# Optimization experiments

Measured on AMD Instinct MI355X. Metric: run time of the kernel, lower is better.

## Reference

```python
import jax, jax.numpy as jnp
import numpy as np

N_TOKENS = 8192
D_MODEL = 1024
HIDDEN = 4096   # d_model * expert_hidden_mult(4)
N_EXPERTS = 8
TOP_K = 2
LN_EPS = 1e-5


def setup_inputs() -> dict:
    key = jax.random.key(0)
    ks = jax.random.split(key, 8)
    s_in = 1.0 / np.sqrt(D_MODEL)
    s_h = 1.0 / np.sqrt(HIDDEN)
    return {
        "x": jax.random.normal(ks[0], (N_TOKENS, D_MODEL), jnp.float32),
        "Wr": jax.random.normal(ks[1], (D_MODEL, N_EXPERTS), jnp.float32) * s_in,
        "W1": jax.random.normal(ks[2], (N_EXPERTS, D_MODEL, HIDDEN), jnp.float32) * s_in,
        "b1": jnp.zeros((N_EXPERTS, HIDDEN), jnp.float32),
        "W2": jax.random.normal(ks[3], (N_EXPERTS, HIDDEN, D_MODEL), jnp.float32) * s_h,
        "b2": jnp.zeros((N_EXPERTS, D_MODEL), jnp.float32),
        "ln_w": jnp.ones((D_MODEL,), jnp.float32),
        "ln_b": jnp.zeros((D_MODEL,), jnp.float32),
    }


def reference(x, Wr, W1, b1, W2, b2, ln_w, ln_b):
    N, d = x.shape
    E = Wr.shape[1]
    # --- Router: top-k softmax gates scattered into dense [N, E] ---
    logits = x @ Wr                                   # [N, E]
    topv, topi = jax.lax.top_k(logits, TOP_K)         # [N, K]
    gv = jax.nn.softmax(topv, axis=-1)                # renormalized top-k gates
    gates = jnp.zeros_like(logits).at[jnp.arange(N)[:, None], topi].set(gv)
    # --- Experts: gate_e > 0 masks tokens; zero gate contributes zero, so
    # dense per-expert FFN weighted by the (mostly-zero) gate column is the
    # same math as the original gather/FFN/scatter-add dispatch. ---
    mixed = jnp.zeros_like(x)
    for e in range(E):  # small fixed expert count
        h = jax.nn.gelu(x @ W1[e] + b1[e])            # [N, HIDDEN]
        y = h @ W2[e] + b2[e]                         # [N, d]
        mixed = mixed + gates[:, e:e + 1] * y
    # --- Load-balancing aux loss (importance * load) ---
    importance = jnp.mean(jax.nn.softmax(logits, axis=-1), axis=0)  # [E]
    load = jnp.mean((gates > 0).astype(x.dtype), axis=0)            # [E]
    aux_loss = E * jnp.sum(importance * load)
    # --- Residual + LayerNorm (output_dropout is identity in eval) ---
    res = x + mixed
    mu = jnp.mean(res, axis=-1, keepdims=True)
    var = jnp.var(res, axis=-1, keepdims=True)
    out = (res - mu) * jax.lax.rsqrt(var + LN_EPS) * ln_w + ln_b
    return out, aux_loss
```

## Files before the change

kernel.cpp:

```cpp
#include <hip/hip_runtime.h>

#define N_TOK 8192
#define DM 1024
#define HID 4096
#define NE 8
#define MAX_TILES 136
#define MAX_SLOTS (MAX_TILES * 128)
#define LN_EPS 1e-5f

typedef __attribute__((ext_vector_type(8))) _Float16 f16x8;
typedef __attribute__((ext_vector_type(4))) _Float16 f16x4;
typedef __attribute__((ext_vector_type(4))) float f32x4;

constexpr size_t OFF_WT1 = 0;
constexpr size_t OFF_WT2 = OFF_WT1 + (size_t)NE * HID * DM * 2;
constexpr size_t OFF_XG  = OFF_WT2 + (size_t)NE * DM * HID * 2;
constexpr size_t OFF_H   = OFF_XG + (size_t)MAX_SLOTS * DM * 2;
constexpr size_t OFF_Y   = OFF_H + (size_t)MAX_SLOTS * HID * 2;
constexpr size_t OFF_TOPI = OFF_Y + (size_t)MAX_SLOTS * DM * 2;
constexpr size_t OFF_TOPG = OFF_TOPI + (size_t)N_TOK * 2 * 4;
constexpr size_t OFF_PTOK = OFF_TOPG + (size_t)N_TOK * 2 * 4;
constexpr size_t OFF_SLOT = OFF_PTOK + (size_t)MAX_SLOTS * 4;
constexpr size_t OFF_HDR = OFF_SLOT + (size_t)N_TOK * 2 * 4;
constexpr size_t WS_NEEDED = OFF_HDR + 4096;

__device__ inline float gelu_tanh(float v) {
  float c = 0.7978845608028654f * (v + 0.044715f * v * v * v);
  return 0.5f * v * (1.0f + tanhf(c));
}

__device__ inline void g2l16(const _Float16* g, _Float16* l) {
  __builtin_amdgcn_global_load_lds(
      (const __attribute__((address_space(1))) unsigned int*)g,
      (__attribute__((address_space(3))) unsigned int*)l, 16, 0, 0);
}

__global__ __launch_bounds__(256) void k_router(
    const float* __restrict__ x, const float* __restrict__ Wr,
    int* __restrict__ topi, float* __restrict__ topg,
    int* __restrict__ cnt, float* __restrict__ imp) {
  __shared__ float wr[DM * NE];
  __shared__ float blkImp[NE];
  __shared__ int blkCnt[NE];
  int tid = threadIdx.x;
  if (tid < NE) { blkImp[tid] = 0.0f; blkCnt[tid] = 0; }
  for (int i = tid; i < DM * NE / 4; i += 256)
    ((float4*)wr)[i] = ((const float4*)Wr)[i];
  __syncthreads();
  int wave = tid >> 6, lane = tid & 63;
  for (int it = 0; it < 4; ++it) {
    int t = blockIdx.x * 16 + wave * 4 + it;
    double acc[NE];
#pragma unroll
    for (int e = 0; e < NE; ++e) acc[e] = 0.0;
    for (int j = 0; j < DM / 64; ++j) {
      int d = j * 64 + lane;
      float xv = x[(size_t)t * DM + d];
#pragma unroll
      for (int e = 0; e < NE; ++e) acc[e] += (double)xv * (double)wr[d * NE + e];
    }
#pragma unroll
    for (int off = 32; off > 0; off >>= 1) {
#pragma unroll
      for (int e = 0; e < NE; ++e) acc[e] += __shfl_down(acc[e], off);
    }
    if (lane == 0) {
      int i0 = 0;
#pragma unroll
      for (int e = 1; e < NE; ++e) if (acc[e] > acc[i0]) i0 = e;
      int i1 = (i0 == 0) ? 1 : 0;
#pragma unroll
      for (int e = 0; e < NE; ++e) if (e != i0 && acc[e] > acc[i1]) i1 = e;
      double g0 = 1.0 / (1.0 + exp(acc[i1] - acc[i0]));
      topi[t * 2] = i0; topi[t * 2 + 1] = i1;
      topg[t * 2] = (float)g0; topg[t * 2 + 1] = (float)(1.0 - g0);
      atomicAdd(&blkCnt[i0], 1); atomicAdd(&blkCnt[i1], 1);
      double mx = acc[0];
#pragma unroll
      for (int e = 1; e < NE; ++e) mx = acc[e] > mx ? acc[e] : mx;
      double s = 0.0, p[NE];
#pragma unroll
      for (int e = 0; e < NE; ++e) { p[e] = exp(acc[e] - mx); s += p[e]; }
      double inv = 1.0 / s;
#pragma unroll
      for (int e = 0; e < NE; ++e) atomicAdd(&blkImp[e], (float)(p[e] * inv));
    }
  }
  __syncthreads();
  if (tid < NE) { atomicAdd(&cnt[tid], blkCnt[tid]); atomicAdd(&imp[tid], blkImp[tid]); }
}

__global__ void k_setup(int* __restrict__ hdr, float* __restrict__ aux_out) {
  int* cnt = hdr;
  float* imp = (float*)(hdr + 8);
  int* cursor = hdr + 16;
  int* off = hdr + 24;
  int* n_tiles_p = hdr + 33;
  int* tile_expert = hdr + 34;
  if (threadIdx.x == 0) {
    int offl[NE + 1];
    int o = 0;
    for (int e = 0; e < NE; ++e) {
      offl[e] = o; off[e] = o; cursor[e] = o;
      o += ((cnt[e] + 127) >> 7) << 7;
    }
    offl[NE] = o; off[NE] = o;
    int nt = o >> 7;
    *n_tiles_p = nt;
    int e = 0;
    for (int i = 0; i < nt; ++i) {
      while (i * 128 >= offl[e + 1]) ++e;
      tile_expert[i] = e;
    }
    double a = 0.0;
    for (int e2 = 0; e2 < NE; ++e2)
      a += ((double)imp[e2] / (double)N_TOK) * ((double)cnt[e2] / (double)N_TOK);
    *aux_out = (float)((double)NE * a);
  }
}

__global__ __launch_bounds__(256) void k_init_pairs(int* __restrict__ pair_token) {
  int i = blockIdx.x * 256 + threadIdx.x;
  if (i < MAX_SLOTS) pair_token[i] = -1;
}

__global__ __launch_bounds__(256) void k_scatter(
    const int* __restrict__ topi, int* __restrict__ cursor,
    int* __restrict__ pair_token, int* __restrict__ slot_of) {
  int t = blockIdx.x * 256 + threadIdx.x;
#pragma unroll
  for (int k = 0; k < 2; ++k) {
    int e = topi[t * 2 + k];
    int p = atomicAdd(&cursor[e], 1);
    pair_token[p] = t;
    slot_of[t * 2 + k] = p;
  }
}

__global__ __launch_bounds__(256) void k_gather(
    const float* __restrict__ x, const int* __restrict__ pair_token,
    _Float16* __restrict__ Xg) {
  int slot = blockIdx.x;
  int t = pair_token[slot];
  int d = threadIdx.x * 4;
  f16x4 v4 = {0, 0, 0, 0};
  if (t >= 0) {
    float4 v = *(const float4*)(x + (size_t)t * DM + d);
    v4[0] = (_Float16)v.x; v4[1] = (_Float16)v.y;
    v4[2] = (_Float16)v.z; v4[3] = (_Float16)v.w;
  }
  *(f16x4*)(Xg + (size_t)slot * DM + d) = v4;
}

__global__ __launch_bounds__(256) void k_transpose(
    const float* __restrict__ in, _Float16* __restrict__ out, int R, int C) {
  __shared__ float tile[32][33];
  size_t base = (size_t)blockIdx.z * R * C;
  const float* src = in + base;
  _Float16* dst = out + base;
  int c0 = blockIdx.x * 32, r0 = blockIdx.y * 32;
  int tx = threadIdx.x & 31, ty = threadIdx.x >> 5;
#pragma unroll
  for (int i = 0; i < 32; i += 8)
    tile[ty + i][tx] = src[(size_t)(r0 + ty + i) * C + c0 + tx];
  __syncthreads();
#pragma unroll
  for (int i = 0; i < 32; i += 8)
    dst[(size_t)(c0 + ty + i) * R + r0 + tx] = (_Float16)tile[tx][ty + i];
}

__device__ inline void stage_async(const _Float16* __restrict__ g, int ld,
                                   _Float16* __restrict__ l, int tid) {
  int wbase = tid & 192;
#pragma unroll
  for (int p = 0; p < 4; ++p) {
    int s = p * 256 + tid;
    int row = s >> 3;
    int c = (s & 7) ^ (row & 7);
    g2l16(g + (size_t)row * ld + c * 8, l + (size_t)(p * 256 + wbase) * 8);
  }
}

__device__ inline f16x8 lds_frag(const _Float16* __restrict__ l, int row, int cc) {
  return *(const f16x8*)(l + row * 64 + (((cc) ^ (row & 7)) << 3));
}

__global__ __launch_bounds__(256, 4) void k_gemm1(
    const _Float16* __restrict__ Xg, const _Float16* __restrict__ Wt1,
    const float* __restrict__ b1, _Float16* __restrict__ H,
    const int* __restrict__ hdr) {
  int tileM = blockIdx.y;
  if (tileM >= hdr[33]) return;
  int e = hdr[34 + tileM];
  int tileN = blockIdx.x;
  __shared__ _Float16 Al[128 * 64];
  __shared__ _Float16 Bl[128 * 64];
  int tid = threadIdx.x;
  const _Float16* Ag = Xg + (size_t)tileM * 128 * DM;
  const _Float16* Bg = Wt1 + (size_t)e * HID * DM + (size_t)tileN * 128 * DM;
  f32x4 acc[4][4];
  const f32x4 fz = {0.f, 0.f, 0.f, 0.f};
#pragma unroll
  for (int a = 0; a < 4; ++a)
#pragma unroll
    for (int b = 0; b < 4; ++b) acc[a][b] = fz;
  int wave = tid >> 6, lane = tid & 63;
  int wm = wave & 1, wn = wave >> 1;
  int l16 = lane & 15, quad = lane >> 4;
  for (int k0 = 0; k0 < DM; k0 += 64) {
    stage_async(Ag + k0, DM, Al, tid);
    stage_async(Bg + k0, DM, Bl, tid);
    __syncthreads();
#pragma unroll
    for (int kk = 0; kk < 64; kk += 32) {
      f16x8 af[4], bfr[4];
      int cc = quad + (kk >> 3);
#pragma unroll
      for (int mi = 0; mi < 4; ++mi)
        af[mi] = lds_frag(Al, wm * 64 + mi * 16 + l16, cc);
#pragma unroll
      for (int ni = 0; ni < 4; ++ni)
        bfr[ni] = lds_frag(Bl, wn * 64 + ni * 16 + l16, cc);
#pragma unroll
      for (int mi = 0; mi < 4; ++mi)
#pragma unroll
        for (int ni = 0; ni < 4; ++ni)
          acc[mi][ni] = __builtin_amdgcn_mfma_f32_16x16x32_f16(af[mi], bfr[ni], acc[mi][ni], 0, 0, 0);
    }
    __syncthreads();
  }
  int rowBase = tileM * 128 + wm * 64;
  int colBase = tileN * 128 + wn * 64;
#pragma unroll
  for (int ni = 0; ni < 4; ++ni) {
    int col = colBase + ni * 16 + l16;
    float bv = b1[e * HID + col];
#pragma unroll
    for (int mi = 0; mi < 4; ++mi)
#pragma unroll
      for (int i = 0; i < 4; ++i) {
        int row = rowBase + mi * 16 + quad * 4 + i;
        float v = acc[mi][ni][i] + bv;
        H[(size_t)row * HID + col] = (_Float16)gelu_tanh(v);
      }
  }
}

__global__ __launch_bounds__(256, 4) void k_gemm2(
    const _Float16* __restrict__ H, const _Float16* __restrict__ Wt2,
    const float* __restrict__ b2, _Float16* __restrict__ Y,
    const int* __restrict__ hdr) {
  int tileM = blockIdx.y;
  if (tileM >= hdr[33]) return;
  int e = hdr[34 + tileM];
  int tileN = blockIdx.x;
  __shared__ _Float16 Al[128 * 64];
  __shared__ _Float16 Bl[128 * 64];
  int tid = threadIdx.x;
  const _Float16* Ag = H + (size_t)tileM * 128 * HID;
  const _Float16* Bg = Wt2 + (size_t)e * DM * HID + (size_t)tileN * 128 * HID;
  f32x4 acc[4][4];
  const f32x4 fz = {0.f, 0.f, 0.f, 0.f};
#pragma unroll
  for (int a = 0; a < 4; ++a)
#pragma unroll
    for (int b = 0; b < 4; ++b) acc[a][b] = fz;
  int wave = tid >> 6, lane = tid & 63;
  int wm = wave & 1, wn = wave >> 1;
  int l16 = lane & 15, quad = lane >> 4;
  for (int k0 = 0; k0 < HID; k0 += 64) {
    stage_async(Ag + k0, HID, Al, tid);
    stage_async(Bg + k0, HID, Bl, tid);
    __syncthreads();
#pragma unroll
    for (int kk = 0; kk < 64; kk += 32) {
      f16x8 af[4], bfr[4];
      int cc = quad + (kk >> 3);
#pragma unroll
      for (int mi = 0; mi < 4; ++mi)
        af[mi] = lds_frag(Al, wm * 64 + mi * 16 + l16, cc);
#pragma unroll
      for (int ni = 0; ni < 4; ++ni)
        bfr[ni] = lds_frag(Bl, wn * 64 + ni * 16 + l16, cc);
#pragma unroll
      for (int mi = 0; mi < 4; ++mi)
#pragma unroll
        for (int ni = 0; ni < 4; ++ni)
          acc[mi][ni] = __builtin_amdgcn_mfma_f32_16x16x32_f16(af[mi], bfr[ni], acc[mi][ni], 0, 0, 0);
    }
    __syncthreads();
  }
  int rowBase = tileM * 128 + wm * 64;
  int colBase = tileN * 128 + wn * 64;
#pragma unroll
  for (int ni = 0; ni < 4; ++ni) {
    int col = colBase + ni * 16 + l16;
    float bv = b2[e * DM + col];
#pragma unroll
    for (int mi = 0; mi < 4; ++mi)
#pragma unroll
      for (int i = 0; i < 4; ++i) {
        int row = rowBase + mi * 16 + quad * 4 + i;
        Y[(size_t)row * DM + col] = (_Float16)(acc[mi][ni][i] + bv);
      }
  }
}

__global__ __launch_bounds__(256) void k_ln(
    const float* __restrict__ x, const _Float16* __restrict__ Y,
    const int* __restrict__ slot_of, const float* __restrict__ topg,
    const float* __restrict__ lnw, const float* __restrict__ lnb,
    float* __restrict__ out) {
  int t = blockIdx.x, tid = threadIdx.x;
  int s0 = slot_of[t * 2], s1 = slot_of[t * 2 + 1];
  float g0 = topg[t * 2], g1 = topg[t * 2 + 1];
  float4 xv = ((const float4*)(x + (size_t)t * DM))[tid];
  f16x4 y0 = ((const f16x4*)(Y + (size_t)s0 * DM))[tid];
  f16x4 y1 = ((const f16x4*)(Y + (size_t)s1 * DM))[tid];
  float r0 = xv.x + g0 * (float)y0[0] + g1 * (float)y1[0];
  float r1 = xv.y + g0 * (float)y0[1] + g1 * (float)y1[1];
  float r2 = xv.z + g0 * (float)y0[2] + g1 * (float)y1[2];
  float r3 = xv.w + g0 * (float)y0[3] + g1 * (float)y1[3];
  float s = r0 + r1 + r2 + r3;
  float s2 = r0 * r0 + r1 * r1 + r2 * r2 + r3 * r3;
#pragma unroll
  for (int off = 32; off > 0; off >>= 1) {
    s += __shfl_down(s, off);
    s2 += __shfl_down(s2, off);
  }
  __shared__ float ss[4], ss2[4];
  int wave = tid >> 6, lane = tid & 63;
  if (lane == 0) { ss[wave] = s; ss2[wave] = s2; }
  __syncthreads();
  float S = ss[0] + ss[1] + ss[2] + ss[3];
  float S2 = ss2[0] + ss2[1] + ss2[2] + ss2[3];
  float mu = S * (1.0f / DM);
  float var = S2 * (1.0f / DM) - mu * mu;
  float inv = rsqrtf(var + LN_EPS);
  float4 wv = ((const float4*)lnw)[tid];
  float4 bv = ((const float4*)lnb)[tid];
  float4 o;
  o.x = (r0 - mu) * inv * wv.x + bv.x;
  o.y = (r1 - mu) * inv * wv.y + bv.y;
  o.z = (r2 - mu) * inv * wv.z + bv.z;
  o.w = (r3 - mu) * inv * wv.w + bv.w;
  ((float4*)(out + (size_t)t * DM))[tid] = o;
}

__global__ void k_sentinel(float* out, float v) { out[threadIdx.x] = v; }

extern "C" void kernel_launch(void* const* d_in, const int* in_sizes, int n_in,
                              void* d_out, int out_size, void* d_ws, size_t ws_size,
                              hipStream_t stream) {
  const float* x = (const float*)d_in[0];
  const float* Wr = (const float*)d_in[1];
  const float* W1 = (const float*)d_in[2];
  const float* b1 = (const float*)d_in[3];
  const float* W2 = (const float*)d_in[4];
  const float* b2 = (const float*)d_in[5];
  const float* lnw = (const float*)d_in[6];
  const float* lnb = (const float*)d_in[7];
  float* out = (float*)d_out;
  char* ws = (char*)d_ws;

  if (ws_size < WS_NEEDED) {
    k_sentinel<<<1, 256, 0, stream>>>(out, 1.0e6f + (float)(ws_size >> 20));
    return;
  }

  _Float16* Wt1 = (_Float16*)(ws + OFF_WT1);
  _Float16* Wt2 = (_Float16*)(ws + OFF_WT2);
  _Float16* Xg = (_Float16*)(ws + OFF_XG);
  _Float16* Hbuf = (_Float16*)(ws + OFF_H);
  _Float16* Ybuf = (_Float16*)(ws + OFF_Y);
  int* topi = (int*)(ws + OFF_TOPI);
  float* topg = (float*)(ws + OFF_TOPG);
  int* pair_token = (int*)(ws + OFF_PTOK);
  int* slot_of = (int*)(ws + OFF_SLOT);
  int* hdr = (int*)(ws + OFF_HDR);
  int* cnt = hdr;
  float* imp = (float*)(hdr + 8);
  int* cursor = hdr + 16;

  hipMemsetAsync(hdr, 0, 64, stream);

  k_transpose<<<dim3(HID / 32, DM / 32, NE), 256, 0, stream>>>(W1, Wt1, DM, HID);
  k_transpose<<<dim3(DM / 32, HID / 32, NE), 256, 0, stream>>>(W2, Wt2, HID, DM);
  k_router<<<512, 256, 0, stream>>>(x, Wr, topi, topg, cnt, imp);
  k_setup<<<1, 1, 0, stream>>>(hdr, out + (size_t)N_TOK * DM);
  k_init_pairs<<<(MAX_SLOTS + 255) / 256, 256, 0, stream>>>(pair_token);
  k_scatter<<<N_TOK / 256, 256, 0, stream>>>(topi, cursor, pair_token, slot_of);
  k_gather<<<MAX_SLOTS, 256, 0, stream>>>(x, pair_token, Xg);
  k_gemm1<<<dim3(HID / 128, MAX_TILES), 256, 0, stream>>>(Xg, Wt1, b1, Hbuf, hdr);
  k_gemm2<<<dim3(DM / 128, MAX_TILES), 256, 0, stream>>>(Hbuf, Wt2, b2, Ybuf, hdr);
  k_ln<<<N_TOK, 256, 0, stream>>>(x, Ybuf, slot_of, topg, lnw, lnb, out);
}
```

Baseline: 870.7 us.

## Vectorize weight transpose, stage GEMM epilogues through LDS, use exp-based GELU

The weight transpose now works on 64x64 tiles, reading with float4 loads and writing 16-byte packed fp16 rows, so the per-call conversion of W1 and W2 should use less bandwidth. Both GEMM epilogues first write their results into per-wave LDS scratch, reusing the staging buffer, and then store 16-byte coalesced rows to H and Y instead of scattered 2-byte stores. GELU's tanh is rewritten as a logistic with __expf, which is mathematically equivalent but may differ slightly in rounding.

```diff
diff --git a/kernel.cpp b/kernel.cpp
--- a/kernel.cpp
+++ b/kernel.cpp
@@ -24,9 +24,9 @@
 constexpr size_t OFF_HDR = OFF_SLOT + (size_t)N_TOK * 2 * 4;
 constexpr size_t WS_NEEDED = OFF_HDR + 4096;
 
-__device__ inline float gelu_tanh(float v) {
+__device__ inline float gelu_fast(float v) {
   float c = 0.7978845608028654f * (v + 0.044715f * v * v * v);
-  return 0.5f * v * (1.0f + tanhf(c));
+  return v / (1.0f + __expf(-2.0f * c));
 }
 
 __device__ inline void g2l16(const _Float16* g, _Float16* l) {
@@ -154,19 +154,27 @@
 
 __global__ __launch_bounds__(256) void k_transpose(
     const float* __restrict__ in, _Float16* __restrict__ out, int R, int C) {
-  __shared__ float tile[32][33];
+  __shared__ float t[64 * 65];
   size_t base = (size_t)blockIdx.z * R * C;
-  const float* src = in + base;
-  _Float16* dst = out + base;
-  int c0 = blockIdx.x * 32, r0 = blockIdx.y * 32;
-  int tx = threadIdx.x & 31, ty = threadIdx.x >> 5;
-#pragma unroll
-  for (int i = 0; i < 32; i += 8)
-    tile[ty + i][tx] = src[(size_t)(r0 + ty + i) * C + c0 + tx];
-  __syncthreads();
-#pragma unroll
-  for (int i = 0; i < 32; i += 8)
-    dst[(size_t)(c0 + ty + i) * R + r0 + tx] = (_Float16)tile[tx][ty + i];
+  int c0 = blockIdx.x * 64, r0 = blockIdx.y * 64;
+  int cx = (threadIdx.x & 15) * 4, ry = threadIdx.x >> 4;
+#pragma unroll
+  for (int p = 0; p < 4; ++p) {
+    int r = p * 16 + ry;
+    float4 v = *(const float4*)(in + base + (size_t)(r0 + r) * C + c0 + cx);
+    t[r * 65 + cx] = v.x; t[r * 65 + cx + 1] = v.y;
+    t[r * 65 + cx + 2] = v.z; t[r * 65 + cx + 3] = v.w;
+  }
+  __syncthreads();
+#pragma unroll
+  for (int q = 0; q < 2; ++q) {
+    int lin = q * 256 + threadIdx.x;
+    int c = lin >> 3, ch = lin & 7;
+    f16x8 v;
+#pragma unroll
+    for (int j = 0; j < 8; ++j) v[j] = (_Float16)t[(ch * 8 + j) * 65 + c];
+    *(f16x8*)(out + base + (size_t)(c0 + c) * R + r0 + ch * 8) = v;
+  }
 }
 
 __device__ inline void stage_async(const _Float16* __restrict__ g, int ld,
@@ -193,8 +201,9 @@
   if (tileM >= hdr[33]) return;
   int e = hdr[34 + tileM];
   int tileN = blockIdx.x;
-  __shared__ _Float16 Al[128 * 64];
-  __shared__ _Float16 Bl[128 * 64];
+  __shared__ _Float16 lds[2 * 128 * 64];
+  _Float16* Al = lds;
+  _Float16* Bl = lds + 128 * 64;
   int tid = threadIdx.x;
   const _Float16* Ag = Xg + (size_t)tileM * 128 * DM;
   const _Float16* Bg = Wt1 + (size_t)e * HID * DM + (size_t)tileN * 128 * DM;
@@ -231,18 +240,27 @@
   }
   int rowBase = tileM * 128 + wm * 64;
   int colBase = tileN * 128 + wn * 64;
-#pragma unroll
-  for (int ni = 0; ni < 4; ++ni) {
-    int col = colBase + ni * 16 + l16;
-    float bv = b1[e * HID + col];
-#pragma unroll
-    for (int mi = 0; mi < 4; ++mi)
+  _Float16* sc = lds + wave * 4096;
+  float bv[4];
+#pragma unroll
+  for (int ni = 0; ni < 4; ++ni) bv[ni] = b1[e * HID + colBase + ni * 16 + l16];
+#pragma unroll
+  for (int mi = 0; mi < 4; ++mi)
+#pragma unroll
+    for (int ni = 0; ni < 4; ++ni)
 #pragma unroll
       for (int i = 0; i < 4; ++i) {
-        int row = rowBase + mi * 16 + quad * 4 + i;
-        float v = acc[mi][ni][i] + bv;
-        H[(size_t)row * HID + col] = (_Float16)gelu_tanh(v);
+        int r = mi * 16 + quad * 4 + i;
+        int c = ni * 16 + l16;
+        sc[r * 64 + c] = (_Float16)gelu_fast(acc[mi][ni][i] + bv[ni]);
       }
+  __syncthreads();
+#pragma unroll
+  for (int j = 0; j < 8; ++j) {
+    int lin = j * 64 + lane;
+    int r = lin >> 3, ch = lin & 7;
+    f16x8 v = *(const f16x8*)(sc + r * 64 + ch * 8);
+    *(f16x8*)(H + (size_t)(rowBase + r) * HID + colBase + ch * 8) = v;
   }
 }
 
@@ -254,8 +272,9 @@
   if (tileM >= hdr[33]) return;
   int e = hdr[34 + tileM];
   int tileN = blockIdx.x;
-  __shared__ _Float16 Al[128 * 64];
-  __shared__ _Float16 Bl[128 * 64];
+  __shared__ _Float16 lds[2 * 128 * 64];
+  _Float16* Al = lds;
+  _Float16* Bl = lds + 128 * 64;
   int tid = threadIdx.x;
   const _Float16* Ag = H + (size_t)tileM * 128 * HID;
   const _Float16* Bg = Wt2 + (size_t)e * DM * HID + (size_t)tileN * 128 * HID;
@@ -292,17 +311,27 @@
   }
   int rowBase = tileM * 128 + wm * 64;
   int colBase = tileN * 128 + wn * 64;
-#pragma unroll
-  for (int ni = 0; ni < 4; ++ni) {
-    int col = colBase + ni * 16 + l16;
-    float bv = b2[e * DM + col];
-#pragma unroll
-    for (int mi = 0; mi < 4; ++mi)
+  _Float16* sc = lds + wave * 4096;
+  float bv[4];
+#pragma unroll
+  for (int ni = 0; ni < 4; ++ni) bv[ni] = b2[e * DM + colBase + ni * 16 + l16];
+#pragma unroll
+  for (int mi = 0; mi < 4; ++mi)
+#pragma unroll
+    for (int ni = 0; ni < 4; ++ni)
 #pragma unroll
       for (int i = 0; i < 4; ++i) {
-        int row = rowBase + mi * 16 + quad * 4 + i;
-        Y[(size_t)row * DM + col] = (_Float16)(acc[mi][ni][i] + bv);
+        int r = mi * 16 + quad * 4 + i;
+        int c = ni * 16 + l16;
+        sc[r * 64 + c] = (_Float16)(acc[mi][ni][i] + bv[ni]);
       }
+  __syncthreads();
+#pragma unroll
+  for (int j = 0; j < 8; ++j) {
+    int lin = j * 64 + lane;
+    int r = lin >> 3, ch = lin & 7;
+    f16x8 v = *(const f16x8*)(sc + r * 64 + ch * 8);
+    *(f16x8*)(Y + (size_t)(rowBase + r) * DM + colBase + ch * 8) = v;
   }
 }
 
@@ -384,8 +413,8 @@
 
   hipMemsetAsync(hdr, 0, 64, stream);
 
-  k_transpose<<<dim3(HID / 32, DM / 32, NE), 256, 0, stream>>>(W1, Wt1, DM, HID);
-  k_transpose<<<dim3(DM / 32, HID / 32, NE), 256, 0, stream>>>(W2, Wt2, HID, DM);
+  k_transpose<<<dim3(HID / 64, DM / 64, NE), 256, 0, stream>>>(W1, Wt1, DM, HID);
+  k_transpose<<<dim3(DM / 64, HID / 64, NE), 256, 0, stream>>>(W2, Wt2, HID, DM);
   k_router<<<512, 256, 0, stream>>>(x, Wr, topi, topg, cnt, imp);
   k_setup<<<1, 1, 0, stream>>>(hdr, out + (size_t)N_TOK * DM);
   k_init_pairs<<<(MAX_SLOTS + 255) / 256, 256, 0, stream>>>(pair_token);
```

New measurement: 841.9 us. 1.03x faster.
